# Kernel optimization log

Measured on AMD Instinct MI355X. Metric: run time of the kernel, lower is better.

Reference implementation:

```python
import jax, jax.numpy as jnp
import numpy as np

# ---- module config (init kwargs) ----
EMB = 256
HIDDEN = 256
L, H, P = 4, 8, 4
CH = HIDDEN // H
PADDING_MODE = "zeros"   # 'zeros' or 'border'
ALIGN_CORNERS = False
# feature pyramid level shapes (height, width), static
SHAPES = np.array([[128, 128], [64, 64], [32, 32], [16, 16]], dtype=np.int32)
LEVEL_STARTS = np.concatenate([[0], np.cumsum(SHAPES.prod(-1))[:-1]]).astype(np.int32)

B, N = 8, 1024
I = int(SHAPES.prod(-1).sum())  # 21760


def setup_inputs() -> dict:
    key = jax.random.key(0)
    ks = jax.random.split(key, 8)
    scale = 0.02
    return {
        "img": jax.random.normal(ks[0], (B, I, EMB), jnp.float32),
        "img_shapes": jnp.asarray(SHAPES),
        "queries": jax.random.normal(ks[1], (B, N, EMB), jnp.float32),
        "reference_points": jax.random.uniform(ks[2], (B, N, 2), dtype=jnp.float32),
        "W_img": jax.random.normal(ks[3], (EMB, HIDDEN), jnp.float32) * scale,
        "b_img": jnp.zeros((HIDDEN,), jnp.float32),
        "W_q": jax.random.normal(ks[4], (EMB, H * L * P * 3), jnp.float32) * scale,
        "b_q": jnp.zeros((H * L * P * 3,), jnp.float32),
        "W_out": jax.random.normal(ks[5], (HIDDEN, EMB), jnp.float32) * scale,
        "b_out": jnp.zeros((EMB,), jnp.float32),
    }


def _msda(img, points, attn):
    """Multiscale deformable attention core.
    img:    [B, I, H, CH] flattened pyramid features
    points: [B, N, H, L, P, 2] (x, y) in [0, 1]
    attn:   [B, N, H, L, P]
    returns [B, N, H, CH]
    """
    b, _, h_, ch = img.shape
    n = points.shape[1]
    img_t = img.transpose(0, 2, 1, 3)  # [B, H, I, CH]
    levels = []
    for l in range(L):
        hh, ww = int(SHAPES[l, 0]), int(SHAPES[l, 1])
        start = int(LEVEL_STARTS[l])
        p = points[:, :, :, l]  # [B, N, H, P, 2]
        # grid_sample pixel mapping (after the module's 2*p-1 normalization)
        if ALIGN_CORNERS:
            x = p[..., 0] * (ww - 1)
            y = p[..., 1] * (hh - 1)
        else:
            x = p[..., 0] * ww - 0.5
            y = p[..., 1] * hh - 0.5
        x0 = jnp.floor(x); y0 = jnp.floor(y)
        wx = x - x0;       wy = y - y0
        x0i = x0.astype(jnp.int32); y0i = y0.astype(jnp.int32)
        acc = jnp.zeros((b, h_, n * P, ch), img.dtype)
        corners = [
            (x0i,     y0i,     (1 - wx) * (1 - wy)),
            (x0i + 1, y0i,     wx * (1 - wy)),
            (x0i,     y0i + 1, (1 - wx) * wy),
            (x0i + 1, y0i + 1, wx * wy),
        ]
        for xi, yi, cw in corners:
            if PADDING_MODE == "zeros":
                valid = (xi >= 0) & (xi < ww) & (yi >= 0) & (yi < hh)
                cw = cw * valid.astype(cw.dtype)
            xc = jnp.clip(xi, 0, ww - 1)
            yc = jnp.clip(yi, 0, hh - 1)
            idx = start + yc * ww + xc                              # [B, N, H, P]
            idx_t = idx.transpose(0, 2, 1, 3).reshape(b, h_, n * P)  # [B, H, N*P]
            g = jnp.take_along_axis(img_t, idx_t[..., None], axis=2)  # [B, H, N*P, CH]
            cw_t = cw.transpose(0, 2, 1, 3).reshape(b, h_, n * P, 1)
            acc = acc + cw_t * g
        levels.append(acc.reshape(b, h_, n, P, ch))
    samples = jnp.stack(levels, axis=3)            # [B, H, N, L, P, CH]
    attn_t = attn.transpose(0, 2, 1, 3, 4)          # [B, H, N, L, P]
    return jnp.einsum("bhnlpc,bhnlp->bnhc", samples, attn_t)


def reference(img, img_shapes, queries, reference_points, W_img, b_img, W_q, b_q, W_out, b_out):
    b, i_, _ = img.shape
    n = queries.shape[1]
    qp = (queries @ W_q + b_q).reshape(b, n, H, L, P, 3)
    offsets = qp[..., :2]                            # [B, N, H, L, P, 2]
    attn = jax.nn.softmax(qp[..., 2].reshape(b, n, H, L * P), axis=-1).reshape(b, n, H, L, P)
    img_p = (img @ W_img + b_img).reshape(b, i_, H, CH)
    shapes_f = img_shapes.astype(jnp.float32)        # [L, 2] (h, w)
    # faithful to source: offsets / img_shapes[:, None, :]
    sampling_points = reference_points[:, :, None, None, None, :] + offsets / shapes_f[:, None, :]
    out = _msda(img_p, sampling_points, attn)        # [B, N, H, CH]
    return out.reshape(b, n, HIDDEN) @ W_out + b_out
```

## Files before the change

### kernel.cpp

```cpp
#include <hip/hip_runtime.h>
#include <type_traits>
#include <utility>

#define B_    8
#define NQ_   1024
#define I_    21760
#define EMB_  256
#define HID_  256
#define H_    8
#define CH_   32

typedef float  f32x4  __attribute__((ext_vector_type(4)));
typedef __bf16 bf16x8 __attribute__((ext_vector_type(8)));
typedef short  s16x8  __attribute__((ext_vector_type(8)));

template <typename V, typename = void>
struct bf16_mfma_native : std::false_type {};
template <typename V>
struct bf16_mfma_native<V, std::void_t<decltype(__builtin_amdgcn_mfma_f32_16x16x32_bf16(
    std::declval<V>(), std::declval<V>(), std::declval<f32x4>(), 0, 0, 0))>>
    : std::true_type {};

template <typename V>
__device__ __forceinline__ f32x4 mfma_dispatch(V a, V b, f32x4 c) {
  if constexpr (bf16_mfma_native<V>::value) {
    return __builtin_amdgcn_mfma_f32_16x16x32_bf16(a, b, c, 0, 0, 0);
  } else {
    return __builtin_amdgcn_mfma_f32_16x16x32_bf16(
        __builtin_bit_cast(s16x8, a), __builtin_bit_cast(s16x8, b), c, 0, 0, 0);
  }
}

__device__ __forceinline__ f32x4 MFMA(s16x8 a, s16x8 b, f32x4 c) {
  return mfma_dispatch(__builtin_bit_cast(bf16x8, a), __builtin_bit_cast(bf16x8, b), c);
}

__device__ __forceinline__ unsigned short f2bf(float f) {
  unsigned u = __float_as_uint(f);
  u += 0x7fffu + ((u >> 16) & 1u);
  return (unsigned short)(u >> 16);
}

template <int NS, int OUTM>
__device__ __forceinline__ void gemm_phase(
    const float* __restrict__ A, const float* __restrict__ W,
    const float* __restrict__ bias, void* __restrict__ Out,
    const int N, const int Mtiles, short* __restrict__ lds,
    const int bid0, const int nblk) {
  const int tid  = threadIdx.x;
  const int lane = tid & 63;
  const int wave = tid >> 6;
  const int quad = lane >> 4;
  const int ln   = lane & 15;

  s16x8 bfrag[NS][8];
  float bv[NS];
#pragma unroll
  for (int st = 0; st < NS; ++st) {
    const int ng = st * 128 + wave * 16 + ln;
    bv[st] = bias[ng];
#pragma unroll
    for (int ks = 0; ks < 8; ++ks) {
      s16x8 f;
#pragma unroll
      for (int j = 0; j < 8; ++j)
        f[j] = (short)f2bf(W[(ks * 32 + quad * 8 + j) * N + ng]);
      bfrag[st][ks] = f;
    }
  }

  const int sr = tid >> 4;
  const int sc = (tid & 15) * 16;

  int t = bid0;
  if (t >= Mtiles) { return; }

  float4 v0, v1, v2, v3;
  {
    const float4* src = (const float4*)(A + ((size_t)t * 32 + sr) * 256 + sc);
    v0 = src[0]; v1 = src[1]; v2 = src[2]; v3 = src[3];
    s16x8 p0, p1;
    p0[0] = (short)f2bf(v0.x); p0[1] = (short)f2bf(v0.y);
    p0[2] = (short)f2bf(v0.z); p0[3] = (short)f2bf(v0.w);
    p0[4] = (short)f2bf(v1.x); p0[5] = (short)f2bf(v1.y);
    p0[6] = (short)f2bf(v1.z); p0[7] = (short)f2bf(v1.w);
    p1[0] = (short)f2bf(v2.x); p1[1] = (short)f2bf(v2.y);
    p1[2] = (short)f2bf(v2.z); p1[3] = (short)f2bf(v2.w);
    p1[4] = (short)f2bf(v3.x); p1[5] = (short)f2bf(v3.y);
    p1[6] = (short)f2bf(v3.z); p1[7] = (short)f2bf(v3.w);
    *(s16x8*)&lds[sr * 264 + sc]     = p0;
    *(s16x8*)&lds[sr * 264 + sc + 8] = p1;
  }
  __syncthreads();

  int cur = 0;
  for (; t < Mtiles; t += nblk) {
    const int tn = t + nblk;
    if (tn < Mtiles) {
      const float4* src = (const float4*)(A + ((size_t)tn * 32 + sr) * 256 + sc);
      v0 = src[0]; v1 = src[1]; v2 = src[2]; v3 = src[3];
    }

    short* buf = lds + cur * (32 * 264);
    f32x4 acc[NS][2];
#pragma unroll
    for (int st = 0; st < NS; ++st) {
      acc[st][0] = f32x4{bv[st], bv[st], bv[st], bv[st]};
      acc[st][1] = acc[st][0];
    }
#pragma unroll
    for (int ks = 0; ks < 8; ++ks) {
      s16x8 a0 = *(const s16x8*)&buf[ln * 264 + ks * 32 + quad * 8];
      s16x8 a1 = *(const s16x8*)&buf[(ln + 16) * 264 + ks * 32 + quad * 8];
#pragma unroll
      for (int st = 0; st < NS; ++st) {
        acc[st][0] = MFMA(a0, bfrag[st][ks], acc[st][0]);
        acc[st][1] = MFMA(a1, bfrag[st][ks], acc[st][1]);
      }
    }

    const size_t rowBase = (size_t)t * 32;
    if constexpr (OUTM == 1) {
      const int tb  = (int)(rowBase / I_);
      const int ir0 = (int)(rowBase - (size_t)tb * I_);
      unsigned short* O = (unsigned short*)Out;
#pragma unroll
      for (int st = 0; st < NS; ++st) {
        const int ng = st * 128 + wave * 16 + ln;
        const int hh = ng >> 5, cc = ng & 31;
        const size_t pl = (size_t)(tb * 8 + hh) * I_;
#pragma unroll
        for (int rt = 0; rt < 2; ++rt) {
#pragma unroll
          for (int r = 0; r < 4; ++r) {
            const size_t i = pl + (size_t)(ir0 + rt * 16 + quad * 4 + r);
            O[i * 32 + cc] = f2bf(acc[st][rt][r]);
          }
        }
      }
    } else {
      float* O = (float*)Out;
#pragma unroll
      for (int st = 0; st < NS; ++st) {
        const int ng = st * 128 + wave * 16 + ln;
#pragma unroll
        for (int rt = 0; rt < 2; ++rt) {
#pragma unroll
          for (int r = 0; r < 4; ++r) {
            const size_t m = rowBase + rt * 16 + quad * 4 + r;
            O[m * N + ng] = acc[st][rt][r];
          }
        }
      }
    }

    if (tn < Mtiles) {
      short* nbuf = lds + (cur ^ 1) * (32 * 264);
      s16x8 p0, p1;
      p0[0] = (short)f2bf(v0.x); p0[1] = (short)f2bf(v0.y);
      p0[2] = (short)f2bf(v0.z); p0[3] = (short)f2bf(v0.w);
      p0[4] = (short)f2bf(v1.x); p0[5] = (short)f2bf(v1.y);
      p0[6] = (short)f2bf(v1.z); p0[7] = (short)f2bf(v1.w);
      p1[0] = (short)f2bf(v2.x); p1[1] = (short)f2bf(v2.y);
      p1[2] = (short)f2bf(v2.z); p1[3] = (short)f2bf(v2.w);
      p1[4] = (short)f2bf(v3.x); p1[5] = (short)f2bf(v3.y);
      p1[6] = (short)f2bf(v3.z); p1[7] = (short)f2bf(v3.w);
      *(s16x8*)&nbuf[sr * 264 + sc]     = p0;
      *(s16x8*)&nbuf[sr * 264 + sc + 8] = p1;
    }
    __syncthreads();
    cur ^= 1;
  }
}

__global__ __launch_bounds__(512, 4) void proj_kernel(
    const float* __restrict__ img, const float* __restrict__ queries,
    const float* __restrict__ W_img, const float* __restrict__ b_img,
    const float* __restrict__ W_q, const float* __restrict__ b_q,
    const float* __restrict__ W_out,
    unsigned short* __restrict__ imgp, float* __restrict__ qp,
    unsigned short* __restrict__ wob) {
  __shared__ __align__(16) short lds[2 * 32 * 264];
  if (blockIdx.x < 448) {
    gemm_phase<2, 1>(img, W_img, b_img, (void*)imgp, 256, (B_ * I_) / 32,
                     lds, blockIdx.x, 448);
  } else {
    gemm_phase<3, 0>(queries, W_q, b_q, (void*)qp, 384, (B_ * NQ_) / 32,
                     lds, (int)blockIdx.x - 448, 64);
    const int t2 = ((int)blockIdx.x - 448) * 512 + (int)threadIdx.x;
    const int col = t2 >> 7;
    const int k   = (t2 << 1) & 255;
    const unsigned lo = f2bf(W_out[(size_t)k * 256 + col]);
    const unsigned hi = f2bf(W_out[(size_t)(k + 1) * 256 + col]);
    ((unsigned*)wob)[t2] = lo | (hi << 16);
  }
}

__global__ __launch_bounds__(256) void msda_out_kernel(
    const unsigned int* __restrict__ imgp,
    const float* __restrict__ qp, const float* __restrict__ refp,
    const unsigned short* __restrict__ wob, const float* __restrict__ b_out,
    float* __restrict__ out) {
  __shared__ __align__(16) float sw[1024][4];
  __shared__ __align__(16) int   sib[1024][2];
  __shared__ __align__(16) short lA[16 * 264];
  const int blk = blockIdx.x;
  const int b   = blk & 7;
  const int n0  = (blk >> 3) << 4;
  const int tid = threadIdx.x;

  for (int half = 0; half < 2; ++half) {
#pragma unroll
    for (int it = 0; it < 4; ++it) {
      const int item = it * 256 + tid;
      const int lp = item & 15, gh = item >> 4;
      const int q8 = gh >> 3, h = gh & 7;
      const int l = lp >> 2;
      const int ww = 128 >> l;
      const int start = (65536 - (65536 >> (2 * l))) / 3;
      const float invsh = __uint_as_float((unsigned)(120 + l) << 23);

      const int n   = n0 + (half << 3) + q8;
      const int bid = (b << 10) | n;
      const float* qb = qp + (size_t)bid * 384 + h * 48 + lp * 3;
      const float ox = qb[0], oy = qb[1], z = qb[2];
      float m = z;
      m = fmaxf(m, __shfl_xor(m, 1, 16));
      m = fmaxf(m, __shfl_xor(m, 2, 16));
      m = fmaxf(m, __shfl_xor(m, 4, 16));
      m = fmaxf(m, __shfl_xor(m, 8, 16));
      float e = __expf(z - m);
      float s = e;
      s += __shfl_xor(s, 1, 16);
      s += __shfl_xor(s, 2, 16);
      s += __shfl_xor(s, 4, 16);
      s += __shfl_xor(s, 8, 16);
      const float a = e / s;

      const float rx = refp[bid * 2], ry = refp[bid * 2 + 1];
      const float px = (rx + ox * invsh) * (float)ww - 0.5f;
      const float py = (ry + oy * invsh) * (float)ww - 0.5f;
      const float x0f = floorf(px), y0f = floorf(py);
      const float wx = px - x0f, wy = py - y0f;
      const int x0 = (int)x0f, y0 = (int)y0f;

      const int xb = min(max(x0, 0), ww - 2);
      float u0 = 0.f, u1 = 0.f;
      if (x0 >= 0 && x0 < ww)         { if (x0 == xb)     u0 += 1.f - wx; else u1 += 1.f - wx; }
      if (x0 + 1 >= 0 && x0 + 1 < ww) { if (x0 + 1 == xb) u0 += wx;       else u1 += wx; }
      const float wy0 = (y0 >= 0     && y0 < ww)     ? a * (1.f - wy) : 0.f;
      const float wy1 = (y0 + 1 >= 0 && y0 + 1 < ww) ? a * wy         : 0.f;
      const int yc0 = min(max(y0, 0), ww - 1);
      const int yc1 = min(max(y0 + 1, 0), ww - 1);

      const int pb = (b * 8 + h) * I_ + start + xb;
      sw[item][0] = wy0 * u0; sw[item][1] = wy0 * u1;
      sw[item][2] = wy1 * u0; sw[item][3] = wy1 * u1;
      sib[item][0] = (pb + yc0 * ww) * 16;
      sib[item][1] = (pb + yc1 * ww) * 16;
    }
    __syncthreads();

#pragma unroll
    for (int it = 0; it < 4; ++it) {
      const int item = it * 256 + tid;
      const int c2 = item & 15, gh = item >> 4;
      const int q8 = gh >> 3, h = gh & 7;
      const int p  = c2 >> 3;
      const int cp = ((c2 & 7) << 1) + (p << 4);
      float a0 = 0.f, a1 = 0.f, a2 = 0.f, a3 = 0.f;
#pragma unroll
      for (int lp = 0; lp < 16; ++lp) {
        const float4 w4 = *(const float4*)sw[gh * 16 + lp];
        const int2   ib = *(const int2*)sib[gh * 16 + lp];
        const float w0 = p ? w4.y : w4.x;
        const float w1 = p ? w4.w : w4.z;
        const uint2 ua = *(const uint2*)&imgp[ib.x + cp];
        const uint2 ub = *(const uint2*)&imgp[ib.y + cp];
        a0 += w0 * __uint_as_float(ua.x << 16);
        a1 += w0 * __uint_as_float(ua.x & 0xffff0000u);
        a2 += w0 * __uint_as_float(ua.y << 16);
        a3 += w0 * __uint_as_float(ua.y & 0xffff0000u);
        a0 += w1 * __uint_as_float(ub.x << 16);
        a1 += w1 * __uint_as_float(ub.x & 0xffff0000u);
        a2 += w1 * __uint_as_float(ub.y << 16);
        a3 += w1 * __uint_as_float(ub.y & 0xffff0000u);
      }
      a0 += __shfl_xor(a0, 8);
      a1 += __shfl_xor(a1, 8);
      a2 += __shfl_xor(a2, 8);
      a3 += __shfl_xor(a3, 8);
      const float rx = p ? a2 : a0;
      const float ry = p ? a3 : a1;
      const int row = (half << 3) + q8;
      const unsigned pr = (unsigned)f2bf(rx) | ((unsigned)f2bf(ry) << 16);
      *(unsigned*)&lA[row * 264 + h * 32 + ((c2 & 7) << 2) + (p << 1)] = pr;
    }
    __syncthreads();
  }

  const int lane = tid & 63, wv = tid >> 6;
  const int quad = lane >> 4, ln = lane & 15;
  f32x4 acc[4];
#pragma unroll
  for (int s = 0; s < 4; ++s) {
    const float bb = b_out[wv * 64 + s * 16 + ln];
    acc[s] = f32x4{bb, bb, bb, bb};
  }
#pragma unroll
  for (int ks = 0; ks < 8; ++ks) {
    const s16x8 a = *(const s16x8*)&lA[ln * 264 + ks * 32 + quad * 8];
#pragma unroll
    for (int s = 0; s < 4; ++s) {
      const int ng = wv * 64 + s * 16 + ln;
      const s16x8 wf = *(const s16x8*)&wob[(size_t)ng * 256 + ks * 32 + quad * 8];
      acc[s] = MFMA(a, wf, acc[s]);
    }
  }
#pragma unroll
  for (int s = 0; s < 4; ++s) {
    const int ng = wv * 64 + s * 16 + ln;
#pragma unroll
    for (int r = 0; r < 4; ++r) {
      const int m = quad * 4 + r;
      out[(size_t)(b * 1024 + n0 + m) * 256 + ng] = acc[s][r];
    }
  }
}

#define OFF_IMGP 0ULL
#define OFF_QP   89128960ULL
#define OFF_WOB  101711872ULL
#define WS_NEEDED 101842944ULL

extern "C" void kernel_launch(void* const* d_in, const int* in_sizes, int n_in,
                              void* d_out, int out_size, void* d_ws, size_t ws_size,
                              hipStream_t stream) {
  const float* img     = (const float*)d_in[0];
  const float* queries = (const float*)d_in[2];
  const float* refp    = (const float*)d_in[3];
  const float* W_img   = (const float*)d_in[4];
  const float* b_img   = (const float*)d_in[5];
  const float* W_q     = (const float*)d_in[6];
  const float* b_q     = (const float*)d_in[7];
  const float* W_out   = (const float*)d_in[8];
  const float* b_out   = (const float*)d_in[9];

  if (ws_size < WS_NEEDED) return;

  char* ws = (char*)d_ws;
  unsigned short* imgp = (unsigned short*)(ws + OFF_IMGP);
  float* qp            = (float*)(ws + OFF_QP);
  unsigned short* wob  = (unsigned short*)(ws + OFF_WOB);

  hipLaunchKernelGGL(proj_kernel, dim3(512), dim3(512), 0, stream,
                     img, queries, W_img, b_img, W_q, b_q, W_out,
                     imgp, qp, wob);
  hipLaunchKernelGGL(msda_out_kernel, dim3(512), dim3(256), 0, stream,
                     (const unsigned int*)imgp, qp, refp, wob, b_out,
                     (float*)d_out);
}
```

Baseline: 330.1 us.

## Pre-convert weights to bf16 in a separate kernel and stream B fragments from memory

Adds a small kernel that converts W_img, W_q and W_out to transposed bf16 once per call. The projection GEMM then loads weight fragments from that global buffer inside the k-loop instead of holding them in registers after a strided per-block fp32 conversion. This lowers register pressure, so the occupancy hint is dropped and the image-projection grid grows from 448 to 704 blocks. The cost is an extra kernel launch and repeated weight-fragment loads in the inner loop, which should mostly hit cache.

New measurement: 323.4 us. 1.02x faster.

```diff
diff --git a/kernel.cpp b/kernel.cpp
--- a/kernel.cpp
+++ b/kernel.cpp
@@ -41,9 +41,26 @@
   return (unsigned short)(u >> 16);
 }
 
+__global__ __launch_bounds__(512) void convert_w(
+    const float* __restrict__ Wi, const float* __restrict__ Wq,
+    const float* __restrict__ Wo, unsigned* __restrict__ wib,
+    unsigned* __restrict__ wqb, unsigned* __restrict__ wob) {
+  const int g = blockIdx.x * 512 + threadIdx.x;
+  const float* S;
+  unsigned* D;
+  int N, t;
+  if (g < 32768)      { S = Wi; D = wib; N = 256; t = g; }
+  else if (g < 81920) { S = Wq; D = wqb; N = 384; t = g - 32768; }
+  else                { S = Wo; D = wob; N = 256; t = g - 81920; }
+  const int col = t >> 7, k = (t & 127) << 1;
+  const unsigned lo = f2bf(S[(size_t)k * N + col]);
+  const unsigned hi = f2bf(S[(size_t)(k + 1) * N + col]);
+  D[t] = lo | (hi << 16);
+}
+
 template <int NS, int OUTM>
 __device__ __forceinline__ void gemm_phase(
-    const float* __restrict__ A, const float* __restrict__ W,
+    const float* __restrict__ A, const unsigned short* __restrict__ Wb,
     const float* __restrict__ bias, void* __restrict__ Out,
     const int N, const int Mtiles, short* __restrict__ lds,
     const int bid0, const int nblk) {
@@ -53,21 +70,11 @@
   const int quad = lane >> 4;
   const int ln   = lane & 15;
 
-  s16x8 bfrag[NS][8];
   float bv[NS];
 #pragma unroll
-  for (int st = 0; st < NS; ++st) {
-    const int ng = st * 128 + wave * 16 + ln;
-    bv[st] = bias[ng];
-#pragma unroll
-    for (int ks = 0; ks < 8; ++ks) {
-      s16x8 f;
-#pragma unroll
-      for (int j = 0; j < 8; ++j)
-        f[j] = (short)f2bf(W[(ks * 32 + quad * 8 + j) * N + ng]);
-      bfrag[st][ks] = f;
-    }
-  }
+  for (int st = 0; st < NS; ++st) bv[st] = bias[st * 128 + wave * 16 + ln];
+
+  const unsigned short* wbase = Wb + (size_t)(wave * 16 + ln) * 256 + quad * 8;
 
   const int sr = tid >> 4;
   const int sc = (tid & 15) * 16;
@@ -114,8 +121,9 @@
       s16x8 a1 = *(const s16x8*)&buf[(ln + 16) * 264 + ks * 32 + quad * 8];
 #pragma unroll
       for (int st = 0; st < NS; ++st) {
-        acc[st][0] = MFMA(a0, bfrag[st][ks], acc[st][0]);
-        acc[st][1] = MFMA(a1, bfrag[st][ks], acc[st][1]);
+        const s16x8 wf = *(const s16x8*)&wbase[(size_t)st * 128 * 256 + ks * 32];
+        acc[st][0] = MFMA(a0, wf, acc[st][0]);
+        acc[st][1] = MFMA(a1, wf, acc[st][1]);
       }
     }
 
@@ -173,26 +181,18 @@
   }
 }
 
-__global__ __launch_bounds__(512, 4) void proj_kernel(
+__global__ __launch_bounds__(512) void proj_kernel(
     const float* __restrict__ img, const float* __restrict__ queries,
-    const float* __restrict__ W_img, const float* __restrict__ b_img,
-    const float* __restrict__ W_q, const float* __restrict__ b_q,
-    const float* __restrict__ W_out,
-    unsigned short* __restrict__ imgp, float* __restrict__ qp,
-    unsigned short* __restrict__ wob) {
+    const unsigned short* __restrict__ wib, const float* __restrict__ b_img,
+    const unsigned short* __restrict__ wqb, const float* __restrict__ b_q,
+    unsigned short* __restrict__ imgp, float* __restrict__ qp) {
   __shared__ __align__(16) short lds[2 * 32 * 264];
-  if (blockIdx.x < 448) {
-    gemm_phase<2, 1>(img, W_img, b_img, (void*)imgp, 256, (B_ * I_) / 32,
-                     lds, blockIdx.x, 448);
+  if (blockIdx.x < 704) {
+    gemm_phase<2, 1>(img, wib, b_img, (void*)imgp, 256, (B_ * I_) / 32,
+                     lds, blockIdx.x, 704);
   } else {
-    gemm_phase<3, 0>(queries, W_q, b_q, (void*)qp, 384, (B_ * NQ_) / 32,
-                     lds, (int)blockIdx.x - 448, 64);
-    const int t2 = ((int)blockIdx.x - 448) * 512 + (int)threadIdx.x;
-    const int col = t2 >> 7;
-    const int k   = (t2 << 1) & 255;
-    const unsigned lo = f2bf(W_out[(size_t)k * 256 + col]);
-    const unsigned hi = f2bf(W_out[(size_t)(k + 1) * 256 + col]);
-    ((unsigned*)wob)[t2] = lo | (hi << 16);
+    gemm_phase<3, 0>(queries, wqb, b_q, (void*)qp, 384, (B_ * NQ_) / 32,
+                     lds, (int)blockIdx.x - 704, 64);
   }
 }
 
@@ -330,8 +330,10 @@
 
 #define OFF_IMGP 0ULL
 #define OFF_QP   89128960ULL
-#define OFF_WOB  101711872ULL
-#define WS_NEEDED 101842944ULL
+#define OFF_WIB  101711872ULL
+#define OFF_WQB  101842944ULL
+#define OFF_WOB  102039552ULL
+#define WS_NEEDED 102170624ULL
 
 extern "C" void kernel_launch(void* const* d_in, const int* in_sizes, int n_in,
                               void* d_out, int out_size, void* d_ws, size_t ws_size,
@@ -351,11 +353,15 @@
   char* ws = (char*)d_ws;
   unsigned short* imgp = (unsigned short*)(ws + OFF_IMGP);
   float* qp            = (float*)(ws + OFF_QP);
+  unsigned short* wib  = (unsigned short*)(ws + OFF_WIB);
+  unsigned short* wqb  = (unsigned short*)(ws + OFF_WQB);
   unsigned short* wob  = (unsigned short*)(ws + OFF_WOB);
 
-  hipLaunchKernelGGL(proj_kernel, dim3(512), dim3(512), 0, stream,
-                     img, queries, W_img, b_img, W_q, b_q, W_out,
-                     imgp, qp, wob);
+  hipLaunchKernelGGL(convert_w, dim3(224), dim3(512), 0, stream,
+                     W_img, W_q, W_out,
+                     (unsigned*)wib, (unsigned*)wqb, (unsigned*)wob);
+  hipLaunchKernelGGL(proj_kernel, dim3(768), dim3(512), 0, stream,
+                     img, queries, wib, b_img, wqb, b_q, imgp, qp);
   hipLaunchKernelGGL(msda_out_kernel, dim3(512), dim3(256), 0, stream,
                      (const unsigned int*)imgp, qp, refp, wob, b_out,
                      (float*)d_out);
```
